# Optimization experiments

Hardware: AMD Instinct MI355X
Metric: run time of the kernel (lower is better)

## Reference

```python
import jax, jax.numpy as jnp
import numpy as np

B, T, F = 256, 128, 256          # batch, input_len, feature_num (= input_size)
HID = [1024, 256]                # hidden_size per layer; HID[-1] must equal F
OUT_LEN = 12
NUM_LAYERS = 2


def setup_inputs() -> dict:
    key = jax.random.key(0)
    ks = jax.random.split(key, 16)
    ins = [F] + HID
    d = {"x": jax.random.normal(ks[0], (B, T, F), dtype=jnp.float32)}
    # Gate order along leading axis 0: [i, f, o, c]
    for j in range(NUM_LAYERS):
        si = 1.0 / np.sqrt(ins[j])
        sh = 1.0 / np.sqrt(HID[j])
        d[f"Wx{j}"] = jax.random.uniform(ks[1 + 4 * j], (4, ins[j], HID[j]), jnp.float32, -si, si)
        d[f"bx{j}"] = jax.random.uniform(ks[2 + 4 * j], (4, HID[j]), jnp.float32, -si, si)
        d[f"Wh{j}"] = jax.random.uniform(ks[3 + 4 * j], (4, HID[j], HID[j]), jnp.float32, -sh, sh)
        d[f"bh{j}"] = jax.random.uniform(ks[4 + 4 * j], (4, HID[j]), jnp.float32, -sh, sh)
    st = 1.0 / np.sqrt(T)
    d["Wout"] = jax.random.uniform(ks[10], (T, OUT_LEN), jnp.float32, -st, st)
    d["bout"] = jax.random.uniform(ks[11], (OUT_LEN,), jnp.float32, -st, st)
    return d


def _lstm_forward(x, Wx, bx, Wh, bh):
    """Stacked LSTM over time. x: (B,T,F). Returns (out_seq (B,T,HID[-1]), h_n list, c_n list)."""
    b = x.shape[0]
    h0 = tuple(jnp.zeros((b, h), x.dtype) for h in HID)
    c0 = tuple(jnp.zeros((b, h), x.dtype) for h in HID)

    def step(carry, x_t):
        hs, cs = carry
        inp = x_t
        new_hs, new_cs = [], []
        for j in range(NUM_LAYERS):
            # fused 4-gate matmuls: (B,in) x (4,in,H) -> (4,B,H)
            g = (jnp.einsum('bi,gih->gbh', inp, Wx[j]) + bx[j][:, None, :]
                 + jnp.einsum('bh,gho->gbo', hs[j], Wh[j]) + bh[j][:, None, :])
            it = jax.nn.sigmoid(g[0])
            ft = jax.nn.sigmoid(g[1])
            ot = jax.nn.sigmoid(g[2])
            c = ft * cs[j] + it * jnp.tanh(g[3])
            h = ot * jnp.tanh(c)
            new_hs.append(h)
            new_cs.append(c)
            inp = h
        return (tuple(new_hs), tuple(new_cs)), inp

    (h_n, c_n), out_seq = jax.lax.scan(step, (h0, c0), jnp.swapaxes(x, 0, 1))
    return jnp.swapaxes(out_seq, 0, 1), h_n, c_n  # (B,T,HID[-1])


def reference(x, Wx0, bx0, Wh0, bh0, Wx1, bx1, Wh1, bh1, Wout, bout):
    Wx = [Wx0, Wx1]; bx = [bx0, bx1]; Wh = [Wh0, Wh1]; bh = [bh0, bh1]
    out_seq, h_n, c_n = _lstm_forward(x, Wx, bx, Wh, bh)
    b = x.shape[0]
    # Faithful to torch: flat row-major view (B,T,F) -> (B,F,T), NOT a transpose
    out = out_seq.reshape(b, -1, T)                 # (B, F, T)
    out = out @ Wout + bout                          # (B, F, OUT_LEN)
    out = out.reshape(b, OUT_LEN, -1)                # (B, OUT_LEN, F)
    return (out, h_n[0], h_n[1], c_n[0], c_n[1])
```

## Files before the change

### kernel.cpp

```cpp
#include <hip/hip_runtime.h>
#include <hip/hip_bf16.h>

typedef unsigned short u16;
typedef unsigned int u32;
typedef unsigned long long u64;
typedef __attribute__((ext_vector_type(8))) short short8;
typedef __attribute__((ext_vector_type(4))) float f32x4;

#define NB 256
#define NT 512
#define TS 128

#define OFF_H0  786432
#define OFF_H1  1048576
#define OFF_C0  1114112
#define OFF_C1  1376256

#define WSO_W0F  0
#define WSO_W1F  (WSO_W0F + 10485760)
#define WSO_B0   (WSO_W1F + 2621440)
#define WSO_B1   (WSO_B0  + 16384)
#define WSO_BAR  (WSO_B1  + 4096)
#define BAR_DW   (4096 + 64)
#define WSO_H0   (WSO_BAR + BAR_DW*4)
#define H0SEQ_BYTES (129*524288)
#define WSO_H1   (WSO_H0 + H0SEQ_BYTES)
#define H1SEQ_BYTES (129*131072)
#define WS_NEED  (WSO_H1 + H1SEQ_BYTES)

#define LDS_XB   65536
#define LDS_B1   98304
#define LDS_SZ   139264

struct MP {
  const float* x;
  const u16*  W0F;
  const u16*  W1F;
  const float* b0;
  const float* b1;
  u16*  H0;
  u16*  H1;
  float* out;
  unsigned* bar;
};

__device__ __forceinline__ float sigm(float x){ return 1.f/(1.f+__expf(-x)); }
__device__ __forceinline__ float tanh_(float x){
  float t = __expf(-2.f*fabsf(x));
  float r = (1.f - t)/(1.f + t);
  return x < 0.f ? -r : r;
}
__device__ __forceinline__ u16 f2b(float v){
  __hip_bfloat16 h = __float2bfloat16(v);
  return *reinterpret_cast<u16*>(&h);
}
__device__ __forceinline__ float b2f(u16 u){
  u32 w = ((u32)u) << 16;
  return *reinterpret_cast<float*>(&w);
}
__device__ __forceinline__ void ast32(u16* p, u32 v){
  __hip_atomic_store((u32*)p, v, __ATOMIC_RELAXED, __HIP_MEMORY_SCOPE_AGENT);
}
__device__ __forceinline__ f32x4 MF(short8 a, short8 b, f32x4 c){
  return __builtin_amdgcn_mfma_f32_16x16x32_bf16(a, b, c, 0, 0, 0);
}
__device__ __forceinline__ void gll16(const void* g, void* l){
  __builtin_amdgcn_global_load_lds(
      (const __attribute__((address_space(1))) void*)g,
      (__attribute__((address_space(3))) void*)l, 16, 0, 0);
}

#define STRX(x) #x
#define PLOADO(dst, ptr, off) asm volatile("global_load_dwordx4 %0, %1, off offset:" STRX(off) : "=v"(dst) : "v"(ptr))
#define VMW(N)  do{ asm volatile("s_waitcnt vmcnt(" STRX(N) ")" ::: "memory"); __builtin_amdgcn_sched_barrier(0); }while(0)
#define BAR     do{ __builtin_amdgcn_s_barrier(); __builtin_amdgcn_sched_barrier(0); }while(0)


__global__ void k_packF0(const float* __restrict__ Wx, const float* __restrict__ Wh,
                         u16* __restrict__ W0F){
  int gid = blockIdx.x*256 + threadIdx.x;
  int F = gid >> 6, lane = gid & 63;
  int kk = F & 3, wn = (F >> 2) & 3;
  int r = F >> 4, kt = r % 10, nt = r / 10;
  int n = nt*64 + wn*16 + (lane & 15);
  int h = n >> 2, g = n & 3;
  int kb = kt*128 + kk*32 + (lane >> 4)*8;
  union { u16 u[8]; short8 v; } pk;
#pragma unroll
  for (int j = 0; j < 8; ++j) {
    int k = kb + j;
    float v = (k < 256) ? Wx[((size_t)g*256 + k)*1024 + h]
                        : Wh[((size_t)g*1024 + (k-256))*1024 + h];
    pk.u[j] = f2b(v);
  }
  *(short8*)&W0F[(size_t)F*512 + lane*8] = pk.v;
}

__global__ void k_packF1(const float* __restrict__ Wx, const float* __restrict__ Wh,
                         u16* __restrict__ W1F){
  int gid = blockIdx.x*256 + threadIdx.x;
  int F = gid >> 6, lane = gid & 63;
  int kk = F & 3, kt = (F >> 2) % 10, ntp = F / 40;
  int n = ntp*16 + (lane & 15);
  int h = n >> 2, g = n & 3;
  int kb = kt*128 + kk*32 + (lane >> 4)*8;
  union { u16 u[8]; short8 v; } pk;
#pragma unroll
  for (int j = 0; j < 8; ++j) {
    int k = kb + j;
    float v = (k < 1024) ? Wx[((size_t)g*1024 + k)*256 + h]
                         : Wh[((size_t)g*256 + (k-1024))*256 + h];
    pk.u[j] = f2b(v);
  }
  *(short8*)&W1F[(size_t)F*512 + lane*8] = pk.v;
}

__global__ void k_bias(const float* __restrict__ bx0, const float* __restrict__ bh0,
                       const float* __restrict__ bx1, const float* __restrict__ bh1,
                       float* __restrict__ b0, float* __restrict__ b1){
  int n = blockIdx.x*256 + threadIdx.x;
  if (n < 4096) { int h = n >> 2, g = n & 3; b0[n] = bx0[g*1024 + h] + bh0[g*1024 + h]; }
  if (n < 1024) { int h = n >> 2, g = n & 3; b1[n] = bx1[g*256 + h] + bh1[g*256 + h]; }
}

__global__ void k_init(u16* __restrict__ H0, u16* __restrict__ H1,
                       unsigned* __restrict__ bar){
  int i = blockIdx.x*256 + threadIdx.x;
  if (i < 262144) H0[i] = 0;
  if (i < 65536)  H1[i] = 0;
  if (i < BAR_DW) bar[i] = 0u;
}


__device__ __forceinline__ void xcvt(const MP& p, int g, char* smem){
  const int tid = threadIdx.x;
  const int row = tid >> 3, f0 = (tid & 7) << 5;
  const int m0 = (blockIdx.x >> 6) << 6;
  const float* xs = p.x + (size_t)(m0 + row)*32768 + (size_t)g*256 + f0;
  f32x4 v0,v1,v2,v3,v4,v5,v6,v7;
  PLOADO(v0, xs, 0);  PLOADO(v1, xs, 16); PLOADO(v2, xs, 32); PLOADO(v3, xs, 48);
  PLOADO(v4, xs, 64); PLOADO(v5, xs, 80); PLOADO(v6, xs, 96); PLOADO(v7, xs, 112);
  VMW(0);
  char* xb = smem + LDS_XB + ((f0 >> 7) << 14);
  const int cb = (f0 & 127) >> 3, sw = row & 7;
  union { u16 u[8]; short8 s; } pk;
#define XPK(VA, VB, CC) \
  pk.u[0]=f2b(VA[0]); pk.u[1]=f2b(VA[1]); pk.u[2]=f2b(VA[2]); pk.u[3]=f2b(VA[3]); \
  pk.u[4]=f2b(VB[0]); pk.u[5]=f2b(VB[1]); pk.u[6]=f2b(VB[2]); pk.u[7]=f2b(VB[3]); \
  *(short8*)(xb + row*256 + ((((cb+(CC)) ^ sw))<<4)) = pk.s;
  XPK(v0,v1,0) XPK(v2,v3,1) XPK(v4,v5,2) XPK(v6,v7,3)
#undef XPK
}

__device__ void phase0(const MP& p, int g, char* smem, float* c0){
  const int bid = blockIdx.x, tid = threadIdx.x;
  const int grp = bid >> 6, nt = bid & 63;
  const int m0 = grp*64, n0 = nt*64;
  const int lane = tid & 63, wid = tid >> 6;
  const int wm = wid >> 2, wn = wid & 3;
  const int lrow = lane & 15, kgrp = lane >> 4;
  const int sw = lrow & 7;
  const int r8 = lane >> 4, c16 = lane & 15;
  const int row0 = wid*8 + r8, row1 = wid*8 + 4 + r8;
  const char* Hp = (const char*)(p.H0 + (size_t)g*262144);
  const char* h0 = Hp + (size_t)(m0+row0)*2048 + ((c16 ^ (row0 & 7))<<4);
  const char* h1 = Hp + (size_t)(m0+row1)*2048 + ((c16 ^ (row1 & 7))<<4);
  char* d0 = smem + wid*2048;
  char* d1 = smem + wid*2048 + 1024;
  const u16* bb = p.W0F + (size_t)nt*81920 + wn*2048 + lane*8;

  short8 bA0,bA1,bA2,bA3, bB0,bB1,bB2,bB3, bC0,bC1,bC2,bC3;
  f32x4 acc0 = {0,0,0,0}, acc1 = {0,0,0,0};

#define P0_B(KT, R0,R1,R2,R3) do{ const u16* _s = bb + (size_t)(KT)*8192; \
    PLOADO(R0,_s,0); PLOADO(R1,_s,1024); PLOADO(R2,_s,2048); PLOADO(R3,_s,3072); }while(0)
#define P0_S(KT) do{ const int _o = ((KT)-2)*256, _bi = (((KT)-2)&3)*16384; \
    gll16(h0 + _o, d0 + _bi); gll16(h1 + _o, d1 + _bi); }while(0)
#define P0_MFB(BP, B0_,B1_,B2_,B3_) do{ const char* _bp = (BP); short8 _a0,_a1; \
    const int _r0 = (wm*32 + lrow)*256, _r1 = _r0 + 16*256; \
    _a0 = *(const short8*)(_bp + _r0 + (((0+kgrp) ^ sw)<<4)); \
    _a1 = *(const short8*)(_bp + _r1 + (((0+kgrp) ^ sw)<<4)); \
    acc0 = MF(_a0,B0_,acc0); acc1 = MF(_a1,B0_,acc1); \
    _a0 = *(const short8*)(_bp + _r0 + (((4+kgrp) ^ sw)<<4)); \
    _a1 = *(const short8*)(_bp + _r1 + (((4+kgrp) ^ sw)<<4)); \
    acc0 = MF(_a0,B1_,acc0); acc1 = MF(_a1,B1_,acc1); \
    _a0 = *(const short8*)(_bp + _r0 + (((8+kgrp) ^ sw)<<4)); \
    _a1 = *(const short8*)(_bp + _r1 + (((8+kgrp) ^ sw)<<4)); \
    acc0 = MF(_a0,B2_,acc0); acc1 = MF(_a1,B2_,acc1); \
    _a0 = *(const short8*)(_bp + _r0 + (((12+kgrp) ^ sw)<<4)); \
    _a1 = *(const short8*)(_bp + _r1 + (((12+kgrp) ^ sw)<<4)); \
    acc0 = MF(_a0,B3_,acc0); acc1 = MF(_a1,B3_,acc1); }while(0)

  P0_B(0, bA0,bA1,bA2,bA3); P0_B(1, bB0,bB1,bB2,bB3); P0_B(2, bC0,bC1,bC2,bC3);
  P0_S(2); P0_S(3); P0_S(4); P0_S(5);
  VMW(16); BAR; P0_MFB(smem + LDS_XB,         bA0,bA1,bA2,bA3); P0_B(3, bA0,bA1,bA2,bA3);
  VMW(16); BAR; P0_MFB(smem + LDS_XB + 16384, bB0,bB1,bB2,bB3); P0_B(4, bB0,bB1,bB2,bB3);
  VMW(14); BAR; P0_MFB(smem,         bC0,bC1,bC2,bC3); P0_B(5, bC0,bC1,bC2,bC3); P0_S(6);
  VMW(10); BAR; P0_MFB(smem + 16384, bA0,bA1,bA2,bA3); P0_B(6, bA0,bA1,bA2,bA3); P0_S(7);
  VMW(12); BAR; P0_MFB(smem + 32768, bB0,bB1,bB2,bB3); P0_B(7, bB0,bB1,bB2,bB3); P0_S(8);
  VMW(14); BAR; P0_MFB(smem + 49152, bC0,bC1,bC2,bC3); P0_B(8, bC0,bC1,bC2,bC3); P0_S(9);
  VMW(14); BAR; P0_MFB(smem,         bA0,bA1,bA2,bA3); P0_B(9, bA0,bA1,bA2,bA3);
  VMW(12); BAR; P0_MFB(smem + 16384, bB0,bB1,bB2,bB3);
  VMW(6);  BAR; P0_MFB(smem + 32768, bC0,bC1,bC2,bC3);
  VMW(0);  BAR; P0_MFB(smem + 49152, bA0,bA1,bA2,bA3);

  __syncthreads();
  float* gl = (float*)smem;
#pragma unroll
  for (int r = 0; r < 4; ++r) {
    gl[(wm*32      + kgrp*4 + r)*68 + wn*16 + lrow] = acc0[r];
    gl[(wm*32 + 16 + kgrp*4 + r)*68 + wn*16 + lrow] = acc1[r];
  }
  __syncthreads();
  u16* H0w = p.H0 + (size_t)(g+1)*262144;
  {
    int bl = tid >> 3, hp = tid & 7;
    int b = m0 + bl, h = nt*16 + hp*2;
    float hn[2];
#pragma unroll
    for (int q = 0; q < 2; ++q) {
      int col = (hp*2 + q)*4;
      float gi = gl[bl*68 + col+0] + p.b0[n0 + col+0];
      float gf = gl[bl*68 + col+1] + p.b0[n0 + col+1];
      float go = gl[bl*68 + col+2] + p.b0[n0 + col+2];
      float gc = gl[bl*68 + col+3] + p.b0[n0 + col+3];
      float cn = sigm(gf)*c0[q] + sigm(gi)*tanh_(gc);
      hn[q] = sigm(go)*tanh_(cn);
      c0[q] = cn;
      if (g == TS-1) {
        p.out[OFF_H0 + (size_t)b*1024 + h + q] = hn[q];
        p.out[OFF_C0 + (size_t)b*1024 + h + q] = cn;
      }
    }
    ast32(H0w + (size_t)b*1024 + h, (u32)f2b(hn[0]) | ((u32)f2b(hn[1]) << 16));
  }
}

__device__ void phase1(const MP& p, int g, char* smem, float* c1){
  const int bid = blockIdx.x, tid = threadIdx.x;
  const int grp = bid >> 6, ntp = bid & 63;
  const int m0 = grp*64, n1 = ntp*16;
  const int lane = tid & 63, wid = tid >> 6;
  const int lrow = lane & 15, kgrp = lane >> 4;
  const int sw = lrow & 7;
  const int r8 = lane >> 4, c16 = lane & 15;
  const int row0 = wid*8 + r8, row1 = wid*8 + 4 + r8;
  const char* HA = (const char*)(p.H0 + (size_t)g*262144);
  const char* HB = (const char*)(p.H1 + (size_t)(g-1)*65536);
  const char* hA0 = HA + (size_t)(m0+row0)*2048 + ((c16 ^ (row0 & 7))<<4);
  const char* hA1 = HA + (size_t)(m0+row1)*2048 + ((c16 ^ (row1 & 7))<<4);
  const char* hB0 = HB + (size_t)(m0+row0)*512  + ((c16 ^ (row0 & 7))<<4);
  const char* hB1 = HB + (size_t)(m0+row1)*512  + ((c16 ^ (row1 & 7))<<4);
  char* d0 = smem + wid*2048;
  char* d1 = smem + wid*2048 + 1024;
  const char* b1p = smem + LDS_B1;
  f32x4 acc = {0,0,0,0};

#define P1_D(KT) do{ const int _bi = ((KT)&3)*16384; \
    if ((KT) < 8) { gll16(hA0 + (KT)*256, d0 + _bi); gll16(hA1 + (KT)*256, d1 + _bi); } \
    else          { gll16(hB0 + ((KT)-8)*256, d0 + _bi); gll16(hB1 + ((KT)-8)*256, d1 + _bi); } }while(0)
#define P1_MF(BUFI, KT) do{ const char* _bp = smem + (BUFI)*16384; \
    const int _ro = (wid*16 + lrow)*256; short8 _a, _b; \
    _a = *(const short8*)(_bp + _ro + (((0+kgrp) ^ sw)<<4)); \
    _b = *(const short8*)(b1p + (((KT)*4+0)<<10) + lane*16); acc = MF(_a,_b,acc); \
    _a = *(const short8*)(_bp + _ro + (((4+kgrp) ^ sw)<<4)); \
    _b = *(const short8*)(b1p + (((KT)*4+1)<<10) + lane*16); acc = MF(_a,_b,acc); \
    _a = *(const short8*)(_bp + _ro + (((8+kgrp) ^ sw)<<4)); \
    _b = *(const short8*)(b1p + (((KT)*4+2)<<10) + lane*16); acc = MF(_a,_b,acc); \
    _a = *(const short8*)(_bp + _ro + (((12+kgrp) ^ sw)<<4)); \
    _b = *(const short8*)(b1p + (((KT)*4+3)<<10) + lane*16); acc = MF(_a,_b,acc); }while(0)

  P1_D(0); P1_D(1); P1_D(2);
  VMW(4); BAR; if (wid < 4) P1_MF(0, 0); P1_D(3);
  VMW(4); BAR; if (wid < 4) P1_MF(1, 1); P1_D(4);
  VMW(4); BAR; if (wid < 4) P1_MF(2, 2); P1_D(5);
  VMW(4); BAR; if (wid < 4) P1_MF(3, 3); P1_D(6);
  VMW(4); BAR; if (wid < 4) P1_MF(0, 4); P1_D(7);
  VMW(4); BAR; if (wid < 4) P1_MF(1, 5); P1_D(8);
  VMW(4); BAR; if (wid < 4) P1_MF(2, 6); P1_D(9);
  VMW(4); BAR; if (wid < 4) P1_MF(3, 7);
  VMW(2); BAR; if (wid < 4) P1_MF(0, 8);
  VMW(0); BAR; if (wid < 4) P1_MF(1, 9);

  __syncthreads();
  float* gl = (float*)smem;
  if (wid < 4) {
#pragma unroll
    for (int r = 0; r < 4; ++r)
      gl[(wid*16 + kgrp*4 + r)*20 + lrow] = acc[r];
  }
  __syncthreads();
  u16* H1w = p.H1 + (size_t)g*65536;
  if (tid < 128) {
    int bl = tid >> 1, hp = tid & 1;
    int b = m0 + bl, h = ntp*4 + hp*2;
    float hn[2];
#pragma unroll
    for (int q = 0; q < 2; ++q) {
      int col = (hp*2 + q)*4;
      float gi = gl[bl*20 + col+0] + p.b1[n1 + col+0];
      float gf = gl[bl*20 + col+1] + p.b1[n1 + col+1];
      float go = gl[bl*20 + col+2] + p.b1[n1 + col+2];
      float gc = gl[bl*20 + col+3] + p.b1[n1 + col+3];
      float cn = sigm(gf)*c1[q] + sigm(gi)*tanh_(gc);
      hn[q] = sigm(go)*tanh_(cn);
      c1[q] = cn;
      if (g == TS) {
        p.out[OFF_H1 + (size_t)b*256 + h + q] = hn[q];
        p.out[OFF_C1 + (size_t)b*256 + h + q] = cn;
      }
    }
    ast32(H1w + (size_t)b*256 + h, (u32)f2b(hn[0]) | ((u32)f2b(hn[1]) << 16));
  }
}

__global__ __launch_bounds__(NT) void k_main(MP p){
  __shared__ __attribute__((aligned(16))) char smem[LDS_SZ];
  float c0[2] = {0.f, 0.f};
  float c1[2] = {0.f, 0.f};
  const int bid = blockIdx.x, tid = threadIdx.x;
  const int grp = bid >> 6, j = bid & 63;
  unsigned* flags = p.bar;
  unsigned* rel   = p.bar + 4096 + grp*16;

  {
    int wid = tid >> 6, lane = tid & 63;
    const char* wsrc = (const char*)p.W1F + (size_t)j*40960 + lane*16;
#pragma unroll
    for (int q = 0; q < 5; ++q) {
      int f = wid*5 + q;
      gll16(wsrc + f*1024, smem + LDS_B1 + f*1024);
    }
    VMW(0);
  }
  xcvt(p, 0, smem);
  __syncthreads();
  phase0(p, 0, smem, c0);

  for (int g = 1; g <= TS; ++g) {
    __syncthreads();
    if (j == 0) {
      if (tid >= 1 && tid < 64) {
        while (__hip_atomic_load(&flags[(grp*64 + tid)*16], __ATOMIC_RELAXED,
                                 __HIP_MEMORY_SCOPE_AGENT) < (unsigned)g)
          __builtin_amdgcn_s_sleep(1);
      }
      __syncthreads();
      if (tid == 0)
        __hip_atomic_store(rel, (unsigned)g, __ATOMIC_RELAXED, __HIP_MEMORY_SCOPE_AGENT);
    } else {
      if (tid == 0)
        __hip_atomic_store(&flags[bid*16], (unsigned)g, __ATOMIC_RELAXED,
                           __HIP_MEMORY_SCOPE_AGENT);
    }
    if (g < TS) xcvt(p, g, smem);
    if (j != 0 && tid == 0) {
      while (__hip_atomic_load(rel, __ATOMIC_RELAXED, __HIP_MEMORY_SCOPE_AGENT) < (unsigned)g)
        __builtin_amdgcn_s_sleep(1);
    }
    __syncthreads();
    phase1(p, g, smem, c1);
    __syncthreads();
    if (g < TS) phase0(p, g, smem, c0);
  }
}

__global__ void k_final_seq(const u16* __restrict__ H1seq, const float* __restrict__ Wout,
                            const float* __restrict__ bout, float* __restrict__ out){
  __shared__ float Ws[1536];
  __shared__ float bs[12];
  for (int i = threadIdx.x; i < 1536; i += 256) Ws[i] = Wout[i];
  if (threadIdx.x < 12) bs[threadIdx.x] = bout[threadIdx.x];
  __syncthreads();
  int gid = blockIdx.x*256 + threadIdx.x;
  int b = gid >> 8, ii = gid & 255;
  const u16* src = H1seq + (size_t)((ii >> 1) + 1)*65536 + b*256 + (ii & 1)*128;
  float acc[12];
#pragma unroll
  for (int k = 0; k < 12; ++k) acc[k] = bs[k];
  for (int jj = 0; jj < 128; jj += 8) {
    union { u16 u[8]; short8 v; } pk;
    pk.v = *(const short8*)&src[jj];
#pragma unroll
    for (int e = 0; e < 8; ++e) {
      float f = b2f(pk.u[e]);
#pragma unroll
      for (int k = 0; k < 12; ++k) acc[k] += f*Ws[(jj+e)*12+k];
    }
  }
  float* dst = out + (size_t)b*3072 + ii*12;
#pragma unroll
  for (int k = 0; k < 12; ++k) dst[k] = acc[k];
}

extern "C" void kernel_launch(void* const* d_in, const int* in_sizes, int n_in,
                              void* d_out, int out_size, void* d_ws, size_t ws_size,
                              hipStream_t stream) {
  if (ws_size < (size_t)WS_NEED) return;
  const float* x    = (const float*)d_in[0];
  const float* Wx0  = (const float*)d_in[1];
  const float* bx0  = (const float*)d_in[2];
  const float* Wh0  = (const float*)d_in[3];
  const float* bh0  = (const float*)d_in[4];
  const float* Wx1  = (const float*)d_in[5];
  const float* bx1  = (const float*)d_in[6];
  const float* Wh1  = (const float*)d_in[7];
  const float* bh1  = (const float*)d_in[8];
  const float* Wout = (const float*)d_in[9];
  const float* bout = (const float*)d_in[10];

  char* ws = (char*)d_ws;
  u16*   W0F  = (u16*)  (ws + WSO_W0F);
  u16*   W1F  = (u16*)  (ws + WSO_W1F);
  float* b0   = (float*)(ws + WSO_B0);
  float* b1   = (float*)(ws + WSO_B1);
  unsigned* bar = (unsigned*)(ws + WSO_BAR);
  u16*   H0   = (u16*)  (ws + WSO_H0);
  u16*   H1   = (u16*)  (ws + WSO_H1);
  float* out = (float*)d_out;

  k_packF0<<<2560, 256, 0, stream>>>(Wx0, Wh0, W0F);
  k_packF1<<<640, 256, 0, stream>>>(Wx1, Wh1, W1F);
  k_bias<<<16, 256, 0, stream>>>(bx0, bh0, bx1, bh1, b0, b1);
  k_init<<<1024, 256, 0, stream>>>(H0, H1, bar);

  MP p;
  p.x = x; p.W0F = W0F; p.W1F = W1F; p.b0 = b0; p.b1 = b1;
  p.H0 = H0; p.H1 = H1; p.out = out; p.bar = bar;
  void* kargs[] = { (void*)&p };
  hipLaunchCooperativeKernel((const void*)k_main, dim3(NB), dim3(NT), kargs, 0, stream);

  k_final_seq<<<256, 256, 0, stream>>>(H1, Wout, bout, out);
}
```

Baseline: 1.487 ms.

## Fuse layer-0 and layer-1 LSTM steps and keep W0 slices register-resident

Merges the separate phase0 and phase1 per-step routines into one fused pass. The staged h0(g) tiles feed both the layer-0 MMA (with register-resident Wh0) and the layer-1 MMA, so H0 is loaded into LDS once per step and one barrier-separated phase disappears. The 32 recurrent-weight fragments (K-tiles 2-9) are preloaded into registers once at kernel start rather than reloaded from global memory every step, with launch_bounds(NT,1) to allow the register budget. This raises register pressure sharply, risks spills, and both epilogues now share LDS regions at different offsets.

```diff
diff --git a/kernel.cpp b/kernel.cpp
--- a/kernel.cpp
+++ b/kernel.cpp
@@ -152,10 +152,12 @@
 #undef XPK
 }
 
-__device__ void phase0(const MP& p, int g, char* smem, float* c0){
+__device__ __forceinline__ void fused(const MP& p, int g, char* smem,
+                                      float* c0, float* c1, short8* wp,
+                                      bool doP0, bool doP1){
   const int bid = blockIdx.x, tid = threadIdx.x;
   const int grp = bid >> 6, nt = bid & 63;
-  const int m0 = grp*64, n0 = nt*64;
+  const int m0 = grp*64, n0 = nt*64, n1 = nt*16;
   const int lane = tid & 63, wid = tid >> 6;
   const int wm = wid >> 2, wn = wid & 3;
   const int lrow = lane & 15, kgrp = lane >> 4;
@@ -165,18 +167,24 @@
   const char* Hp = (const char*)(p.H0 + (size_t)g*262144);
   const char* h0 = Hp + (size_t)(m0+row0)*2048 + ((c16 ^ (row0 & 7))<<4);
   const char* h1 = Hp + (size_t)(m0+row1)*2048 + ((c16 ^ (row1 & 7))<<4);
+  const int gB = (g > 0) ? (g-1) : 0;
+  const char* HB = (const char*)(p.H1 + (size_t)gB*65536);
+  const char* hB0 = HB + (size_t)(m0+row0)*512 + ((c16 ^ (row0 & 7))<<4);
+  const char* hB1 = HB + (size_t)(m0+row1)*512 + ((c16 ^ (row1 & 7))<<4);
   char* d0 = smem + wid*2048;
   char* d1 = smem + wid*2048 + 1024;
   const u16* bb = p.W0F + (size_t)nt*81920 + wn*2048 + lane*8;
-
-  short8 bA0,bA1,bA2,bA3, bB0,bB1,bB2,bB3, bC0,bC1,bC2,bC3;
+  const char* b1p = smem + LDS_B1;
+
+  short8 bx0,bx1,bx2,bx3, by0,by1,by2,by3;
   f32x4 acc0 = {0,0,0,0}, acc1 = {0,0,0,0};
-
-#define P0_B(KT, R0,R1,R2,R3) do{ const u16* _s = bb + (size_t)(KT)*8192; \
-    PLOADO(R0,_s,0); PLOADO(R1,_s,1024); PLOADO(R2,_s,2048); PLOADO(R3,_s,3072); }while(0)
-#define P0_S(KT) do{ const int _o = ((KT)-2)*256, _bi = (((KT)-2)&3)*16384; \
+  f32x4 accp = {0,0,0,0};
+
+#define FS0(T) do{ const int _o = ((T)-2)*256, _bi = (((T)-2)&3)*16384; \
     gll16(h0 + _o, d0 + _bi); gll16(h1 + _o, d1 + _bi); }while(0)
-#define P0_MFB(BP, B0_,B1_,B2_,B3_) do{ const char* _bp = (BP); short8 _a0,_a1; \
+#define FS1(T) do{ const int _o = ((T)-10)*256, _bi = (((T)-2)&3)*16384; \
+    gll16(hB0 + _o, d0 + _bi); gll16(hB1 + _o, d1 + _bi); }while(0)
+#define F_MFB(BP, B0_,B1_,B2_,B3_) do{ const char* _bp = (BP); short8 _a0,_a1; \
     const int _r0 = (wm*32 + lrow)*256, _r1 = _r0 + 16*256; \
     _a0 = *(const short8*)(_bp + _r0 + (((0+kgrp) ^ sw)<<4)); \
     _a1 = *(const short8*)(_bp + _r1 + (((0+kgrp) ^ sw)<<4)); \
@@ -190,40 +198,72 @@
     _a0 = *(const short8*)(_bp + _r0 + (((12+kgrp) ^ sw)<<4)); \
     _a1 = *(const short8*)(_bp + _r1 + (((12+kgrp) ^ sw)<<4)); \
     acc0 = MF(_a0,B3_,acc0); acc1 = MF(_a1,B3_,acc1); }while(0)
-
-  P0_B(0, bA0,bA1,bA2,bA3); P0_B(1, bB0,bB1,bB2,bB3); P0_B(2, bC0,bC1,bC2,bC3);
-  P0_S(2); P0_S(3); P0_S(4); P0_S(5);
-  VMW(16); BAR; P0_MFB(smem + LDS_XB,         bA0,bA1,bA2,bA3); P0_B(3, bA0,bA1,bA2,bA3);
-  VMW(16); BAR; P0_MFB(smem + LDS_XB + 16384, bB0,bB1,bB2,bB3); P0_B(4, bB0,bB1,bB2,bB3);
-  VMW(14); BAR; P0_MFB(smem,         bC0,bC1,bC2,bC3); P0_B(5, bC0,bC1,bC2,bC3); P0_S(6);
-  VMW(10); BAR; P0_MFB(smem + 16384, bA0,bA1,bA2,bA3); P0_B(6, bA0,bA1,bA2,bA3); P0_S(7);
-  VMW(12); BAR; P0_MFB(smem + 32768, bB0,bB1,bB2,bB3); P0_B(7, bB0,bB1,bB2,bB3); P0_S(8);
-  VMW(14); BAR; P0_MFB(smem + 49152, bC0,bC1,bC2,bC3); P0_B(8, bC0,bC1,bC2,bC3); P0_S(9);
-  VMW(14); BAR; P0_MFB(smem,         bA0,bA1,bA2,bA3); P0_B(9, bA0,bA1,bA2,bA3);
-  VMW(12); BAR; P0_MFB(smem + 16384, bB0,bB1,bB2,bB3);
-  VMW(6);  BAR; P0_MFB(smem + 32768, bC0,bC1,bC2,bC3);
-  VMW(0);  BAR; P0_MFB(smem + 49152, bA0,bA1,bA2,bA3);
+#define F_MF1(BUFI, KT1) do{ const char* _bp = smem + (BUFI)*16384; \
+    const int _ro = (wid*16 + lrow)*256; short8 _a, _b; \
+    _a = *(const short8*)(_bp + _ro + (((0+kgrp) ^ sw)<<4)); \
+    _b = *(const short8*)(b1p + (((KT1)*4+0)<<10) + lane*16); accp = MF(_a,_b,accp); \
+    _a = *(const short8*)(_bp + _ro + (((4+kgrp) ^ sw)<<4)); \
+    _b = *(const short8*)(b1p + (((KT1)*4+1)<<10) + lane*16); accp = MF(_a,_b,accp); \
+    _a = *(const short8*)(_bp + _ro + (((8+kgrp) ^ sw)<<4)); \
+    _b = *(const short8*)(b1p + (((KT1)*4+2)<<10) + lane*16); accp = MF(_a,_b,accp); \
+    _a = *(const short8*)(_bp + _ro + (((12+kgrp) ^ sw)<<4)); \
+    _b = *(const short8*)(b1p + (((KT1)*4+3)<<10) + lane*16); accp = MF(_a,_b,accp); }while(0)
+
+  { const u16* _s = bb;
+    PLOADO(bx0,_s,0); PLOADO(bx1,_s,1024); PLOADO(bx2,_s,2048); PLOADO(bx3,_s,3072); }
+  { const u16* _s = bb + 8192;
+    PLOADO(by0,_s,0); PLOADO(by1,_s,1024); PLOADO(by2,_s,2048); PLOADO(by3,_s,3072); }
+  FS0(2); FS0(3); FS0(4); FS0(5);
+
+  VMW(12); BAR; if (doP0) F_MFB(smem + LDS_XB,         bx0,bx1,bx2,bx3);
+  VMW(8);  BAR; if (doP0) F_MFB(smem + LDS_XB + 16384, by0,by1,by2,by3);
+  VMW(6); BAR; if (doP0) F_MFB(smem,         wp[0], wp[1], wp[2], wp[3]);
+               if (doP1 && wid < 4) F_MF1(0, 0);  FS0(6);
+  VMW(6); BAR; if (doP0) F_MFB(smem + 16384, wp[4], wp[5], wp[6], wp[7]);
+               if (doP1 && wid < 4) F_MF1(1, 1);  FS0(7);
+  VMW(6); BAR; if (doP0) F_MFB(smem + 32768, wp[8], wp[9], wp[10], wp[11]);
+               if (doP1 && wid < 4) F_MF1(2, 2);  FS0(8);
+  VMW(6); BAR; if (doP0) F_MFB(smem + 49152, wp[12], wp[13], wp[14], wp[15]);
+               if (doP1 && wid < 4) F_MF1(3, 3);  FS0(9);
+  VMW(6); BAR; if (doP0) F_MFB(smem,         wp[16], wp[17], wp[18], wp[19]);
+               if (doP1 && wid < 4) F_MF1(0, 4);  FS1(10);
+  VMW(6); BAR; if (doP0) F_MFB(smem + 16384, wp[20], wp[21], wp[22], wp[23]);
+               if (doP1 && wid < 4) F_MF1(1, 5);  FS1(11);
+  VMW(6); BAR; if (doP0) F_MFB(smem + 32768, wp[24], wp[25], wp[26], wp[27]);
+               if (doP1 && wid < 4) F_MF1(2, 6);
+  VMW(4); BAR; if (doP0) F_MFB(smem + 49152, wp[28], wp[29], wp[30], wp[31]);
+               if (doP1 && wid < 4) F_MF1(3, 7);
+  VMW(2); BAR; if (doP1 && wid < 4) F_MF1(0, 8);
+  VMW(0); BAR; if (doP1 && wid < 4) F_MF1(1, 9);
 
   __syncthreads();
-  float* gl = (float*)smem;
-#pragma unroll
-  for (int r = 0; r < 4; ++r) {
-    gl[(wm*32      + kgrp*4 + r)*68 + wn*16 + lrow] = acc0[r];
-    gl[(wm*32 + 16 + kgrp*4 + r)*68 + wn*16 + lrow] = acc1[r];
+  float* gl0 = (float*)smem;
+  float* gl1 = (float*)(smem + 20480);
+  if (doP0) {
+#pragma unroll
+    for (int r = 0; r < 4; ++r) {
+      gl0[(wm*32      + kgrp*4 + r)*68 + wn*16 + lrow] = acc0[r];
+      gl0[(wm*32 + 16 + kgrp*4 + r)*68 + wn*16 + lrow] = acc1[r];
+    }
+  }
+  if (doP1 && wid < 4) {
+#pragma unroll
+    for (int r = 0; r < 4; ++r)
+      gl1[(wid*16 + kgrp*4 + r)*20 + lrow] = accp[r];
   }
   __syncthreads();
-  u16* H0w = p.H0 + (size_t)(g+1)*262144;
-  {
+  if (doP0) {
+    u16* H0w = p.H0 + (size_t)(g+1)*262144;
     int bl = tid >> 3, hp = tid & 7;
     int b = m0 + bl, h = nt*16 + hp*2;
     float hn[2];
 #pragma unroll
     for (int q = 0; q < 2; ++q) {
       int col = (hp*2 + q)*4;
-      float gi = gl[bl*68 + col+0] + p.b0[n0 + col+0];
-      float gf = gl[bl*68 + col+1] + p.b0[n0 + col+1];
-      float go = gl[bl*68 + col+2] + p.b0[n0 + col+2];
-      float gc = gl[bl*68 + col+3] + p.b0[n0 + col+3];
+      float gi = gl0[bl*68 + col+0] + p.b0[n0 + col+0];
+      float gf = gl0[bl*68 + col+1] + p.b0[n0 + col+1];
+      float go = gl0[bl*68 + col+2] + p.b0[n0 + col+2];
+      float gc = gl0[bl*68 + col+3] + p.b0[n0 + col+3];
       float cn = sigm(gf)*c0[q] + sigm(gi)*tanh_(gc);
       hn[q] = sigm(go)*tanh_(cn);
       c0[q] = cn;
@@ -234,74 +274,18 @@
     }
     ast32(H0w + (size_t)b*1024 + h, (u32)f2b(hn[0]) | ((u32)f2b(hn[1]) << 16));
   }
-}
-
-__device__ void phase1(const MP& p, int g, char* smem, float* c1){
-  const int bid = blockIdx.x, tid = threadIdx.x;
-  const int grp = bid >> 6, ntp = bid & 63;
-  const int m0 = grp*64, n1 = ntp*16;
-  const int lane = tid & 63, wid = tid >> 6;
-  const int lrow = lane & 15, kgrp = lane >> 4;
-  const int sw = lrow & 7;
-  const int r8 = lane >> 4, c16 = lane & 15;
-  const int row0 = wid*8 + r8, row1 = wid*8 + 4 + r8;
-  const char* HA = (const char*)(p.H0 + (size_t)g*262144);
-  const char* HB = (const char*)(p.H1 + (size_t)(g-1)*65536);
-  const char* hA0 = HA + (size_t)(m0+row0)*2048 + ((c16 ^ (row0 & 7))<<4);
-  const char* hA1 = HA + (size_t)(m0+row1)*2048 + ((c16 ^ (row1 & 7))<<4);
-  const char* hB0 = HB + (size_t)(m0+row0)*512  + ((c16 ^ (row0 & 7))<<4);
-  const char* hB1 = HB + (size_t)(m0+row1)*512  + ((c16 ^ (row1 & 7))<<4);
-  char* d0 = smem + wid*2048;
-  char* d1 = smem + wid*2048 + 1024;
-  const char* b1p = smem + LDS_B1;
-  f32x4 acc = {0,0,0,0};
-
-#define P1_D(KT) do{ const int _bi = ((KT)&3)*16384; \
-    if ((KT) < 8) { gll16(hA0 + (KT)*256, d0 + _bi); gll16(hA1 + (KT)*256, d1 + _bi); } \
-    else          { gll16(hB0 + ((KT)-8)*256, d0 + _bi); gll16(hB1 + ((KT)-8)*256, d1 + _bi); } }while(0)
-#define P1_MF(BUFI, KT) do{ const char* _bp = smem + (BUFI)*16384; \
-    const int _ro = (wid*16 + lrow)*256; short8 _a, _b; \
-    _a = *(const short8*)(_bp + _ro + (((0+kgrp) ^ sw)<<4)); \
-    _b = *(const short8*)(b1p + (((KT)*4+0)<<10) + lane*16); acc = MF(_a,_b,acc); \
-    _a = *(const short8*)(_bp + _ro + (((4+kgrp) ^ sw)<<4)); \
-    _b = *(const short8*)(b1p + (((KT)*4+1)<<10) + lane*16); acc = MF(_a,_b,acc); \
-    _a = *(const short8*)(_bp + _ro + (((8+kgrp) ^ sw)<<4)); \
-    _b = *(const short8*)(b1p + (((KT)*4+2)<<10) + lane*16); acc = MF(_a,_b,acc); \
-    _a = *(const short8*)(_bp + _ro + (((12+kgrp) ^ sw)<<4)); \
-    _b = *(const short8*)(b1p + (((KT)*4+3)<<10) + lane*16); acc = MF(_a,_b,acc); }while(0)
-
-  P1_D(0); P1_D(1); P1_D(2);
-  VMW(4); BAR; if (wid < 4) P1_MF(0, 0); P1_D(3);
-  VMW(4); BAR; if (wid < 4) P1_MF(1, 1); P1_D(4);
-  VMW(4); BAR; if (wid < 4) P1_MF(2, 2); P1_D(5);
-  VMW(4); BAR; if (wid < 4) P1_MF(3, 3); P1_D(6);
-  VMW(4); BAR; if (wid < 4) P1_MF(0, 4); P1_D(7);
-  VMW(4); BAR; if (wid < 4) P1_MF(1, 5); P1_D(8);
-  VMW(4); BAR; if (wid < 4) P1_MF(2, 6); P1_D(9);
-  VMW(4); BAR; if (wid < 4) P1_MF(3, 7);
-  VMW(2); BAR; if (wid < 4) P1_MF(0, 8);
-  VMW(0); BAR; if (wid < 4) P1_MF(1, 9);
-
-  __syncthreads();
-  float* gl = (float*)smem;
-  if (wid < 4) {
-#pragma unroll
-    for (int r = 0; r < 4; ++r)
-      gl[(wid*16 + kgrp*4 + r)*20 + lrow] = acc[r];
-  }
-  __syncthreads();
-  u16* H1w = p.H1 + (size_t)g*65536;
-  if (tid < 128) {
+  if (doP1 && tid < 128) {
+    u16* H1w = p.H1 + (size_t)g*65536;
     int bl = tid >> 1, hp = tid & 1;
-    int b = m0 + bl, h = ntp*4 + hp*2;
+    int b = m0 + bl, h = nt*4 + hp*2;
     float hn[2];
 #pragma unroll
     for (int q = 0; q < 2; ++q) {
       int col = (hp*2 + q)*4;
-      float gi = gl[bl*20 + col+0] + p.b1[n1 + col+0];
-      float gf = gl[bl*20 + col+1] + p.b1[n1 + col+1];
-      float go = gl[bl*20 + col+2] + p.b1[n1 + col+2];
-      float gc = gl[bl*20 + col+3] + p.b1[n1 + col+3];
+      float gi = gl1[bl*20 + col+0] + p.b1[n1 + col+0];
+      float gf = gl1[bl*20 + col+1] + p.b1[n1 + col+1];
+      float go = gl1[bl*20 + col+2] + p.b1[n1 + col+2];
+      float gc = gl1[bl*20 + col+3] + p.b1[n1 + col+3];
       float cn = sigm(gf)*c1[q] + sigm(gi)*tanh_(gc);
       hn[q] = sigm(go)*tanh_(cn);
       c1[q] = cn;
@@ -314,17 +298,18 @@
   }
 }
 
-__global__ __launch_bounds__(NT) void k_main(MP p){
+__global__ __launch_bounds__(NT, 1) void k_main(MP p){
   __shared__ __attribute__((aligned(16))) char smem[LDS_SZ];
   float c0[2] = {0.f, 0.f};
   float c1[2] = {0.f, 0.f};
+  short8 wp[32];
   const int bid = blockIdx.x, tid = threadIdx.x;
   const int grp = bid >> 6, j = bid & 63;
+  const int lane = tid & 63, wid = tid >> 6;
   unsigned* flags = p.bar;
   unsigned* rel   = p.bar + 4096 + grp*16;
 
   {
-    int wid = tid >> 6, lane = tid & 63;
     const char* wsrc = (const char*)p.W1F + (size_t)j*40960 + lane*16;
 #pragma unroll
     for (int q = 0; q < 5; ++q) {
@@ -333,9 +318,19 @@
     }
     VMW(0);
   }
+  {
+    const u16* bb = p.W0F + (size_t)j*81920 + (wid & 3)*2048 + lane*8;
+#define LDW(T) do{ const u16* _s = bb + (size_t)(T)*8192; \
+    PLOADO(wp[((T)-2)*4+0],_s,0); PLOADO(wp[((T)-2)*4+1],_s,1024); \
+    PLOADO(wp[((T)-2)*4+2],_s,2048); PLOADO(wp[((T)-2)*4+3],_s,3072); }while(0)
+    LDW(2); LDW(3); LDW(4); LDW(5); LDW(6); LDW(7); LDW(8); LDW(9);
+#undef LDW
+    VMW(0);
+  }
+
   xcvt(p, 0, smem);
   __syncthreads();
-  phase0(p, 0, smem, c0);
+  fused(p, 0, smem, c0, c1, wp, true, false);
 
   for (int g = 1; g <= TS; ++g) {
     __syncthreads();
@@ -359,9 +354,7 @@
         __builtin_amdgcn_s_sleep(1);
     }
     __syncthreads();
-    phase1(p, g, smem, c1);
-    __syncthreads();
-    if (g < TS) phase0(p, g, smem, c0);
+    fused(p, g, smem, c0, c1, wp, g < TS, true);
   }
 }
 
```

Result: faster. 1.205 ms (-19.0%).
